# Kernel optimization log

Measured on AMD Instinct MI355X. Metric: run time of the kernel, lower is better.

## Reference

```python
import jax, jax.numpy as jnp
import numpy as np

NB_CLASSES = 100000
N_NODES = NB_CLASSES - 1   # internal huffman nodes
INPUT_DIM = 512
BATCH = 1024
NB_REQ = 8
MAX_DEPTH = 17             # ~ceil(log2(nb_classes)) for uniform frequency table


def setup_inputs() -> dict:
    key = jax.random.key(0)
    k1, k2, k3, k4, k5, k6 = jax.random.split(key, 6)
    input_vector = jax.random.normal(k1, (BATCH, INPUT_DIM), dtype=jnp.float32)
    target_classes = jax.random.randint(k2, (BATCH, NB_REQ), 0, NB_CLASSES, dtype=jnp.int32)
    # learned params: W (n_nodes, d), b (n_nodes,)  (trailing singleton dim dropped)
    W = jax.random.normal(k3, (N_NODES, INPUT_DIM), dtype=jnp.float32) * 0.02
    b = jnp.zeros((N_NODES,), dtype=jnp.float32)
    # constant tree tables built at layer-build time: per-class node path + binary code
    class_path_map = jax.random.randint(k4, (NB_CLASSES, MAX_DEPTH), 0, N_NODES, dtype=jnp.int32)
    huffman_codes = jax.random.randint(k5, (NB_CLASSES, MAX_DEPTH), 0, 2, dtype=jnp.int32).astype(jnp.float32)
    return {
        "input_vector": input_vector,
        "target_classes": target_classes,
        "W": W,
        "b": b,
        "class_path_map": class_path_map,
        "huffman_codes": huffman_codes,
    }


def reference(input_vector, target_classes, W, b, class_path_map, huffman_codes):
    # req_nodes: (B, K, D) node indices along the huffman path of each target class
    req_nodes = class_path_map[target_classes]
    # gather per-node weight rows and biases: (B, K, D, d), (B, K, D)
    req_W = W[req_nodes]
    req_b = b[req_nodes]
    # logits: dot of input vector with each gathered node weight row
    y = jnp.einsum('bd,bkcd->bkc', input_vector, req_W) + req_b
    p = jax.nn.sigmoid(y)                     # (B, K, D)
    h = huffman_codes[target_classes]         # (B, K, D) in {0,1}
    # branch prob: p if code==0 else (1-p); padded depths have h=0 -> multiply by p of padded node
    # (matches original: prod(h + p - 2*h*p) over depth)
    return jnp.prod(h + p - 2.0 * h * p, axis=-1)   # (B, K)
```

## Files before the change

### kernel.cpp

```cpp
#include <hip/hip_runtime.h>
#include <math.h>

#define BATCH      1024
#define NB_REQ     8
#define INPUT_DIM  512
#define MAX_DEPTH  17

__global__ __launch_bounds__(256) void huffmax_kernel(
    const float* __restrict__ x,
    const int*   __restrict__ targets,
    const float* __restrict__ W,
    const float* __restrict__ bias,
    const int*   __restrict__ path,
    const float* __restrict__ codes,
    float*       __restrict__ out)
{
    const int wave = threadIdx.x >> 6;
    const int lane = threadIdx.x & 63;
    const int pair = blockIdx.x * 4 + wave;
    if (pair >= BATCH * NB_REQ) return;
    const int bi = pair >> 3;

    const float4* xrow = reinterpret_cast<const float4*>(x + (long)bi * INPUT_DIM);
    const float4 x0 = xrow[lane * 2 + 0];
    const float4 x1 = xrow[lane * 2 + 1];

    const int cls = targets[pair];
    const int*   prow = path  + (long)cls * MAX_DEPTH;
    const float* hrow = codes + (long)cls * MAX_DEPTH;

    float prod = 1.0f;
    for (int d = 0; d < MAX_DEPTH; ++d) {
        const int node = prow[d];
        const float4* wrow =
            reinterpret_cast<const float4*>(W + (long)node * INPUT_DIM);
        const float4 w0 = wrow[lane * 2 + 0];
        const float4 w1 = wrow[lane * 2 + 1];

        float acc = x0.x * w0.x + x0.y * w0.y + x0.z * w0.z + x0.w * w0.w
                  + x1.x * w1.x + x1.y * w1.y + x1.z * w1.z + x1.w * w1.w;

        #pragma unroll
        for (int off = 32; off > 0; off >>= 1)
            acc += __shfl_xor(acc, off, 64);

        const float y = acc + bias[node];
        const float p = 1.0f / (1.0f + expf(-y));
        const float h = hrow[d];
        prod *= (h + p - 2.0f * h * p);
    }

    if (lane == 0) out[pair] = prod;
}

extern "C" void kernel_launch(void* const* d_in, const int* in_sizes, int n_in,
                              void* d_out, int out_size, void* d_ws, size_t ws_size,
                              hipStream_t stream) {
    const float* x       = (const float*)d_in[0];
    const int*   targets = (const int*)  d_in[1];
    const float* W       = (const float*)d_in[2];
    const float* bias    = (const float*)d_in[3];
    const int*   path    = (const int*)  d_in[4];
    const float* codes   = (const float*)d_in[5];
    float*       out     = (float*)d_out;

    const int pairs  = BATCH * NB_REQ;
    const int blocks = pairs / 4;

    huffmax_kernel<<<blocks, 256, 0, stream>>>(x, targets, W, bias, path, codes, out);
}
```

Baseline: 48.28 us.

## Hoist path loads and issue all weight-row gathers before reductions

```diff
diff --git a/kernel.cpp b/kernel.cpp
--- a/kernel.cpp
+++ b/kernel.cpp
@@ -18,36 +18,50 @@
     const int wave = threadIdx.x >> 6;
     const int lane = threadIdx.x & 63;
     const int pair = blockIdx.x * 4 + wave;
-    if (pair >= BATCH * NB_REQ) return;
-    const int bi = pair >> 3;
+    const int bi   = pair >> 3;
 
-    const float4* xrow = reinterpret_cast<const float4*>(x + (long)bi * INPUT_DIM);
+    const float4* xrow = reinterpret_cast<const float4*>(x + (size_t)bi * INPUT_DIM);
     const float4 x0 = xrow[lane * 2 + 0];
     const float4 x1 = xrow[lane * 2 + 1];
 
-    const int cls = targets[pair];
-    const int*   prow = path  + (long)cls * MAX_DEPTH;
-    const float* hrow = codes + (long)cls * MAX_DEPTH;
+    const int cls = __builtin_amdgcn_readfirstlane(targets[pair]);
+
+    int nodes[MAX_DEPTH];
+    #pragma unroll
+    for (int d = 0; d < MAX_DEPTH; ++d)
+        nodes[d] = __builtin_amdgcn_readfirstlane(path[(size_t)cls * MAX_DEPTH + d]);
+
+    float h[MAX_DEPTH];
+    float bv[MAX_DEPTH];
+    #pragma unroll
+    for (int d = 0; d < MAX_DEPTH; ++d) {
+        h[d]  = codes[(size_t)cls * MAX_DEPTH + d];
+        bv[d] = bias[nodes[d]];
+    }
+
+    float acc[MAX_DEPTH];
+    #pragma unroll
+    for (int d = 0; d < MAX_DEPTH; ++d) {
+        const float4* wrow =
+            reinterpret_cast<const float4*>(W + (size_t)nodes[d] * INPUT_DIM);
+        const float4 w0 = wrow[lane * 2 + 0];
+        const float4 w1 = wrow[lane * 2 + 1];
+        acc[d] = x0.x * w0.x + x0.y * w0.y + x0.z * w0.z + x0.w * w0.w
+               + x1.x * w1.x + x1.y * w1.y + x1.z * w1.z + x1.w * w1.w;
+    }
+
+    #pragma unroll
+    for (int off = 32; off >= 1; off >>= 1) {
+        #pragma unroll
+        for (int d = 0; d < MAX_DEPTH; ++d)
+            acc[d] += __shfl_xor(acc[d], off, 64);
+    }
 
     float prod = 1.0f;
+    #pragma unroll
     for (int d = 0; d < MAX_DEPTH; ++d) {
-        const int node = prow[d];
-        const float4* wrow =
-            reinterpret_cast<const float4*>(W + (long)node * INPUT_DIM);
-        const float4 w0 = wrow[lane * 2 + 0];
-        const float4 w1 = wrow[lane * 2 + 1];
-
-        float acc = x0.x * w0.x + x0.y * w0.y + x0.z * w0.z + x0.w * w0.w
-                  + x1.x * w1.x + x1.y * w1.y + x1.z * w1.z + x1.w * w1.w;
-
-        #pragma unroll
-        for (int off = 32; off > 0; off >>= 1)
-            acc += __shfl_xor(acc, off, 64);
-
-        const float y = acc + bias[node];
-        const float p = 1.0f / (1.0f + expf(-y));
-        const float h = hrow[d];
-        prod *= (h + p - 2.0f * h * p);
+        const float p = 1.0f / (1.0f + expf(-(acc[d] + bv[d])));
+        prod *= (h[d] + p - 2.0f * h[d] * p);
     }
 
     if (lane == 0) out[pair] = prod;
```

Measured after the change: 50.54 us. +4.7%, slower.

## Group gathered path nodes by node so each weight row is read once

Applied to the files above, without the earlier changes.

```diff
diff --git a/kernel.cpp b/kernel.cpp
--- a/kernel.cpp
+++ b/kernel.cpp
@@ -1,56 +1,98 @@
 #include <hip/hip_runtime.h>
 #include <math.h>
+#include <stdint.h>
 
 #define BATCH      1024
 #define NB_REQ     8
 #define INPUT_DIM  512
 #define MAX_DEPTH  17
+#define NB_CLASSES 100000
+#define N_NODES    (NB_CLASSES - 1)
+#define ITEMS      (BATCH * NB_REQ * MAX_DEPTH)
+#define CAP        16
 
-__global__ __launch_bounds__(256) void huffmax_kernel(
+
+__global__ __launch_bounds__(256) void zero_kernel(uint32_t* __restrict__ cnt) {
+    const int i = blockIdx.x * 256 + threadIdx.x;
+    if (i < N_NODES) cnt[i] = 0u;
+}
+
+__global__ __launch_bounds__(256) void build_kernel(
+    const int* __restrict__ targets,
+    const int* __restrict__ path,
+    uint32_t*  __restrict__ cnt,
+    uint32_t*  __restrict__ slots)
+{
+    const int t = blockIdx.x * 256 + threadIdx.x;
+    if (t >= ITEMS) return;
+    const int pair = t / MAX_DEPTH;
+    const int d    = t - pair * MAX_DEPTH;
+    const int cls  = targets[pair];
+    const int node = path[(size_t)cls * MAX_DEPTH + d];
+    const uint32_t pos = atomicAdd(&cnt[node], 1u);
+    if (pos < CAP) slots[(size_t)node * CAP + pos] = (uint32_t)t;
+}
+
+__global__ __launch_bounds__(256) void main_kernel(
     const float* __restrict__ x,
     const int*   __restrict__ targets,
     const float* __restrict__ W,
     const float* __restrict__ bias,
-    const int*   __restrict__ path,
     const float* __restrict__ codes,
-    float*       __restrict__ out)
+    const uint32_t* __restrict__ cnt,
+    const uint32_t* __restrict__ slots,
+    float*       __restrict__ fact)
 {
     const int wave = threadIdx.x >> 6;
     const int lane = threadIdx.x & 63;
-    const int pair = blockIdx.x * 4 + wave;
-    if (pair >= BATCH * NB_REQ) return;
-    const int bi = pair >> 3;
+    const int node = blockIdx.x * 4 + wave;
+    if (node >= N_NODES) return;
 
-    const float4* xrow = reinterpret_cast<const float4*>(x + (long)bi * INPUT_DIM);
-    const float4 x0 = xrow[lane * 2 + 0];
-    const float4 x1 = xrow[lane * 2 + 1];
+    const uint32_t c0 = cnt[node];
+    const int c = __builtin_amdgcn_readfirstlane((int)(c0 > CAP ? CAP : c0));
+    if (c == 0) return;
 
-    const int cls = targets[pair];
-    const int*   prow = path  + (long)cls * MAX_DEPTH;
-    const float* hrow = codes + (long)cls * MAX_DEPTH;
+    const float4* wrow = reinterpret_cast<const float4*>(W + (size_t)node * INPUT_DIM);
+    const float4 w0 = wrow[lane * 2 + 0];
+    const float4 w1 = wrow[lane * 2 + 1];
+    const float  bv = bias[node];
 
-    float prod = 1.0f;
-    for (int d = 0; d < MAX_DEPTH; ++d) {
-        const int node = prow[d];
-        const float4* wrow =
-            reinterpret_cast<const float4*>(W + (long)node * INPUT_DIM);
-        const float4 w0 = wrow[lane * 2 + 0];
-        const float4 w1 = wrow[lane * 2 + 1];
+    for (int j = 0; j < c; ++j) {
+        const int t    = __builtin_amdgcn_readfirstlane((int)slots[(size_t)node * CAP + j]);
+        const int pair = t / MAX_DEPTH;
+        const int d    = t - pair * MAX_DEPTH;
+        const int bi   = pair >> 3;
+
+        const float4* xrow = reinterpret_cast<const float4*>(x + (size_t)bi * INPUT_DIM);
+        const float4 x0 = xrow[lane * 2 + 0];
+        const float4 x1 = xrow[lane * 2 + 1];
 
         float acc = x0.x * w0.x + x0.y * w0.y + x0.z * w0.z + x0.w * w0.w
                   + x1.x * w1.x + x1.y * w1.y + x1.z * w1.z + x1.w * w1.w;
 
         #pragma unroll
-        for (int off = 32; off > 0; off >>= 1)
+        for (int off = 32; off >= 1; off >>= 1)
             acc += __shfl_xor(acc, off, 64);
 
-        const float y = acc + bias[node];
-        const float p = 1.0f / (1.0f + expf(-y));
-        const float h = hrow[d];
-        prod *= (h + p - 2.0f * h * p);
+        const int   cls = targets[pair];
+        const float h   = codes[(size_t)cls * MAX_DEPTH + d];
+        const float p   = 1.0f / (1.0f + expf(-(acc + bv)));
+        const float f   = h + p - 2.0f * h * p;
+
+        if (lane == 0) fact[t] = f;
     }
+}
 
-    if (lane == 0) out[pair] = prod;
+__global__ __launch_bounds__(256) void finalize_kernel(
+    const float* __restrict__ fact,
+    float*       __restrict__ out)
+{
+    const int pair = blockIdx.x * 256 + threadIdx.x;
+    float prod = 1.0f;
+    #pragma unroll
+    for (int d = 0; d < MAX_DEPTH; ++d)
+        prod *= fact[(size_t)pair * MAX_DEPTH + d];
+    out[pair] = prod;
 }
 
 extern "C" void kernel_launch(void* const* d_in, const int* in_sizes, int n_in,
@@ -64,8 +106,13 @@
     const float* codes   = (const float*)d_in[5];
     float*       out     = (float*)d_out;
 
-    const int pairs  = BATCH * NB_REQ;
-    const int blocks = pairs / 4;
+    uint32_t* cnt   = (uint32_t*)d_ws;
+    uint32_t* slots = cnt + 100000;
+    float*    fact  = (float*)(slots + (size_t)100000 * CAP);
 
-    huffmax_kernel<<<blocks, 256, 0, stream>>>(x, targets, W, bias, path, codes, out);
+    zero_kernel    <<<(N_NODES + 255) / 256, 256, 0, stream>>>(cnt);
+    build_kernel   <<<(ITEMS + 255) / 256,   256, 0, stream>>>(targets, path, cnt, slots);
+    main_kernel    <<<(N_NODES + 3) / 4,     256, 0, stream>>>(x, targets, W, bias, codes,
+                                                               cnt, slots, fact);
+    finalize_kernel<<<BATCH * NB_REQ / 256,  256, 0, stream>>>(fact, out);
 }
```

New measurement: 67.36 us. 1.4x slower.
